# Optimization experiments

Hardware: AMD Instinct MI355X
Metric: run time of the kernel (lower is better)

## Reference

```python
import jax, jax.numpy as jnp
import numpy as np
from jax import lax

STRIDE = 1
PAD = 1  # module pads 1 on each side whenever padding != 0


def setup_inputs() -> dict:
    key = jax.random.key(0)
    kx, kw, kb = jax.random.split(key, 3)
    x = jax.random.normal(kx, (4096, 4096), dtype=jnp.float32)
    weight = jax.random.normal(kw, (15, 15), dtype=jnp.float32)
    bias = jax.random.normal(kb, (1,), dtype=jnp.float32)
    return {"x": x, "weight": weight, "bias": bias}


def reference(x, weight, bias):
    # Single-channel 2D cross-correlation with constant zero padding of 1 and
    # stride STRIDE, plus a scalar bias. lax.conv_general_dilated computes
    # correlation (no kernel flip), matching the torch corr2d loop exactly.
    out = lax.conv_general_dilated(
        x[None, None, :, :],          # NCHW, N=C=1
        weight[None, None, :, :],      # OIHW, O=I=1
        window_strides=(STRIDE, STRIDE),
        padding=[(PAD, PAD), (PAD, PAD)],
        dimension_numbers=("NCHW", "OIHW", "NCHW"),
    )[0, 0]
    return out + bias[0]
```

## Files before the change

### kernel.cpp

```cpp
#include <hip/hip_runtime.h>

#define IN_N   4096
#define OW     4084
#define KS     15
#define TILE   64
#define XROWS  78
#define XS     88
#define TILES  4
#define NBX    64
#define NBY    16
#define NRT    64

typedef __attribute__((ext_vector_type(8))) short     v8s;
typedef __attribute__((ext_vector_type(8))) _Float16  v8h;
typedef __attribute__((ext_vector_type(4))) float     v4f;
typedef __attribute__((ext_vector_type(2))) float     v2f;
typedef __attribute__((ext_vector_type(4))) unsigned  v4u;

__global__ void build_B(const float* __restrict__ w, unsigned short* __restrict__ Bg) {
    int ky = blockIdx.x;
    int e  = threadIdx.x;
    int n = e & 15, quad = e >> 4;
    unsigned short vals[8];
    #pragma unroll
    for (int j = 0; j < 8; ++j) {
        int d = quad * 8 + j - 1 - n;
        _Float16 h = (_Float16)0.0f;
        if (d >= 0 && d < KS) h = (_Float16)w[ky * KS + d];
        union { _Float16 hh; unsigned short u; } cv; cv.hh = h;
        vals[j] = cv.u;
    }
    *(v8s*)(&Bg[(ky * 64 + e) * 8]) = *(const v8s*)vals;
}

__device__ __forceinline__ unsigned pk(float a, float b) {
    return __builtin_bit_cast(unsigned, __builtin_amdgcn_cvt_pkrtz(a, b));
}

__device__ __forceinline__ void stage_direct(
    const float* __restrict__ x, unsigned short* __restrict__ buf,
    int tid, int R0, int X0, bool fast)
{
    #pragma unroll
    for (int s = 0; s < 4; ++s) {
        int i = s * 256 + tid;
        if (i < XROWS * 10) {
            int row = i / 10, u = i - 10 * row;
            int gr  = R0 - 1 + row;
            int gc0 = X0 - 2 + 8 * u;
            v4u p;
            if (fast) {
                const float* xr = x + (size_t)gr * IN_N + gc0;
                v2f f0 = *(const v2f*)(xr + 0);
                v2f f1 = *(const v2f*)(xr + 2);
                v2f f2 = *(const v2f*)(xr + 4);
                v2f f3 = *(const v2f*)(xr + 6);
                p.x = pk(f0.x, f0.y); p.y = pk(f1.x, f1.y);
                p.z = pk(f2.x, f2.y); p.w = pk(f3.x, f3.y);
            } else {
                float f[8];
                #pragma unroll
                for (int j = 0; j < 8; ++j) f[j] = 0.0f;
                if ((unsigned)gr < (unsigned)IN_N) {
                    const float* xr = x + (size_t)gr * IN_N;
                    #pragma unroll
                    for (int j = 0; j < 8; ++j)
                        if ((unsigned)(gc0 + j) < (unsigned)IN_N) f[j] = xr[gc0 + j];
                }
                p.x = pk(f[0], f[1]); p.y = pk(f[2], f[3]);
                p.z = pk(f[4], f[5]); p.w = pk(f[6], f[7]);
            }
            *(v4u*)(&buf[row * XS + 8 * u]) = p;
        }
    }
}

__device__ __forceinline__ void issue_loads(
    const float* __restrict__ x, int tid, int R0, int X0, v2f L[4][4])
{
    #pragma unroll
    for (int s = 0; s < 4; ++s) {
        int i = s * 256 + tid;
        if (i < XROWS * 10) {
            int row = i / 10, u = i - 10 * row;
            const float* xr = x + (size_t)(R0 - 1 + row) * IN_N + (X0 - 2 + 8 * u);
            L[s][0] = *(const v2f*)(xr + 0);
            L[s][1] = *(const v2f*)(xr + 2);
            L[s][2] = *(const v2f*)(xr + 4);
            L[s][3] = *(const v2f*)(xr + 6);
        }
    }
}

__device__ __forceinline__ void write_held(
    unsigned short* __restrict__ buf, int tid, v2f L[4][4])
{
    #pragma unroll
    for (int s = 0; s < 4; ++s) {
        int i = s * 256 + tid;
        if (i < XROWS * 10) {
            int row = i / 10, u = i - 10 * row;
            v4u p;
            p.x = pk(L[s][0].x, L[s][0].y);
            p.y = pk(L[s][1].x, L[s][1].y);
            p.z = pk(L[s][2].x, L[s][2].y);
            p.w = pk(L[s][3].x, L[s][3].y);
            *(v4u*)(&buf[row * XS + 8 * u]) = p;
        }
    }
}

__global__ __launch_bounds__(256, 3) void conv2d_mfma8(
    const float* __restrict__ x, const unsigned short* __restrict__ Bg,
    const float* __restrict__ bias, float* __restrict__ out)
{
    __shared__ unsigned short xt[2][XROWS * XS] __attribute__((aligned(16)));
    __shared__ unsigned short Bl[KS * 64 * 8]  __attribute__((aligned(16)));

    const int tid = threadIdx.x;
    const int bx = blockIdx.x, by = blockIdx.y;
    const int X0  = bx * TILE;
    const int RT0 = by * TILES;
    const bool colInt = (bx >= 1) & (bx <= NBX - 2);

    {
        const v8s* Bgs = (const v8s*)Bg;
        v8s* Bls = (v8s*)Bl;
        #pragma unroll
        for (int s = 0; s < 4; ++s) {
            int i = s * 256 + tid;
            if (i < KS * 64) Bls[i] = Bgs[i];
        }
    }

    stage_direct(x, xt[0], tid, RT0 * TILE, X0,
                 colInt & (RT0 >= 1) & (RT0 <= NRT - 2));
    __syncthreads();

    const int lane = tid & 63;
    const int wv   = tid >> 6;
    const int m    = lane & 15;
    const int quad = lane >> 4;
    const float bv = bias[0];

    v2f L[4][4];

    #pragma unroll
    for (int t = 0; t < TILES; ++t) {
        const int RT = RT0 + t;
        const int R0 = RT * TILE;
        const unsigned short* cur = xt[t & 1];
        unsigned short* nxt = xt[(t + 1) & 1];
        const bool hasNext = (t < TILES - 1);
        const bool nFast = hasNext & colInt & ((RT + 1) <= NRT - 2);

        if (nFast) issue_loads(x, tid, (RT + 1) * TILE, X0, L);
        __builtin_amdgcn_sched_barrier(0);

        v4f acc[4];
        #pragma unroll
        for (int c = 0; c < 4; ++c) acc[c] = (v4f){0.f, 0.f, 0.f, 0.f};

        const unsigned short* arow = &cur[(wv * 16 + m) * XS + quad * 8];
        #pragma unroll
        for (int ky = 0; ky < KS; ++ky) {
            v8h bf = *(const v8h*)(&Bl[(ky * 64 + lane) * 8]);
            v8h a0 = *(const v8h*)(arow + 0);
            v8h a1 = *(const v8h*)(arow + 16);
            v8h a2 = *(const v8h*)(arow + 32);
            v8h a3 = *(const v8h*)(arow + 48);
            acc[0] = __builtin_amdgcn_mfma_f32_16x16x32_f16(a0, bf, acc[0], 0, 0, 0);
            acc[1] = __builtin_amdgcn_mfma_f32_16x16x32_f16(a1, bf, acc[1], 0, 0, 0);
            acc[2] = __builtin_amdgcn_mfma_f32_16x16x32_f16(a2, bf, acc[2], 0, 0, 0);
            acc[3] = __builtin_amdgcn_mfma_f32_16x16x32_f16(a3, bf, acc[3], 0, 0, 0);
            arow += XS;
        }

        const int orow0 = R0 + wv * 16 + quad * 4;
        const int ocol0 = X0 + m;
        if ((bx < NBX - 1) & (RT < NRT - 1)) {
            float* o0 = &out[(size_t)orow0 * OW + ocol0];
            #pragma unroll
            for (int c = 0; c < 4; ++c) {
                #pragma unroll
                for (int r = 0; r < 4; ++r)
                    o0[(size_t)r * OW + c * 16] = acc[c][r] + bv;
            }
        } else {
            #pragma unroll
            for (int c = 0; c < 4; ++c) {
                int oc = ocol0 + c * 16;
                if (oc < OW) {
                    #pragma unroll
                    for (int r = 0; r < 4; ++r) {
                        int orow = orow0 + r;
                        if (orow < OW)
                            out[(size_t)orow * OW + oc] = acc[c][r] + bv;
                    }
                }
            }
        }
        __builtin_amdgcn_sched_barrier(0);

        if (hasNext) {
            if (nFast) write_held(nxt, tid, L);
            else       stage_direct(x, nxt, tid, (RT + 1) * TILE, X0, false);
        }
        __syncthreads();
    }
}

extern "C" void kernel_launch(void* const* d_in, const int* in_sizes, int n_in,
                              void* d_out, int out_size, void* d_ws, size_t ws_size,
                              hipStream_t stream) {
    const float* x    = (const float*)d_in[0];
    const float* w    = (const float*)d_in[1];
    const float* bias = (const float*)d_in[2];
    float* out        = (float*)d_out;
    unsigned short* Bg = (unsigned short*)d_ws;

    build_B<<<dim3(KS), dim3(64), 0, stream>>>(w, Bg);
    dim3 grid(NBX, NBY);
    conv2d_mfma8<<<grid, dim3(256), 0, stream>>>(x, Bg, bias, out);
}
```

Before: 152.3 us.

## Stage next input tile via global_load_lds DMA into a raw fp32 LDS buffer

Replaces the register-held prefetch of the next input tile with direct global-to-LDS loads into a raw float buffer. After the MFMA loop, a wait and barrier are followed by converting that buffer to fp16 in the single tile buffer. Rows per block are doubled (8 tiles, half the grid) and the row loop is no longer unrolled, which lowers register pressure. The cost is extra LDS traffic, an extra barrier per tile, and less overlap because the conversion is serialized before the next compute. Occupancy drops to 2 blocks per CU.

```diff
diff --git a/kernel.cpp b/kernel.cpp
--- a/kernel.cpp
+++ b/kernel.cpp
@@ -6,15 +6,17 @@
 #define TILE   64
 #define XROWS  78
 #define XS     88
-#define TILES  4
+#define TILES  8
 #define NBX    64
-#define NBY    16
+#define NBY    8
 #define NRT    64
+#define RAWCH  98
 
 typedef __attribute__((ext_vector_type(8))) short     v8s;
 typedef __attribute__((ext_vector_type(8))) _Float16  v8h;
 typedef __attribute__((ext_vector_type(4))) float     v4f;
 typedef __attribute__((ext_vector_type(2))) float     v2f;
+typedef __attribute__((ext_vector_type(2))) unsigned  v2u;
 typedef __attribute__((ext_vector_type(4))) unsigned  v4u;
 
 __global__ void build_B(const float* __restrict__ w, unsigned short* __restrict__ Bg) {
@@ -35,6 +37,12 @@
 
 __device__ __forceinline__ unsigned pk(float a, float b) {
     return __builtin_bit_cast(unsigned, __builtin_amdgcn_cvt_pkrtz(a, b));
+}
+
+__device__ __forceinline__ void gl_lds4(const float* g, float* l) {
+    __builtin_amdgcn_global_load_lds(
+        (const __attribute__((address_space(1))) void*)g,
+        (__attribute__((address_space(3))) void*)l, 4, 0, 0);
 }
 
 __device__ __forceinline__ void stage_direct(
@@ -75,47 +83,48 @@
     }
 }
 
-__device__ __forceinline__ void issue_loads(
-    const float* __restrict__ x, int tid, int R0, int X0, v2f L[4][4])
-{
-    #pragma unroll
-    for (int s = 0; s < 4; ++s) {
-        int i = s * 256 + tid;
-        if (i < XROWS * 10) {
-            int row = i / 10, u = i - 10 * row;
-            const float* xr = x + (size_t)(R0 - 1 + row) * IN_N + (X0 - 2 + 8 * u);
-            L[s][0] = *(const v2f*)(xr + 0);
-            L[s][1] = *(const v2f*)(xr + 2);
-            L[s][2] = *(const v2f*)(xr + 4);
-            L[s][3] = *(const v2f*)(xr + 6);
-        }
-    }
-}
-
-__device__ __forceinline__ void write_held(
-    unsigned short* __restrict__ buf, int tid, v2f L[4][4])
-{
-    #pragma unroll
-    for (int s = 0; s < 4; ++s) {
-        int i = s * 256 + tid;
-        if (i < XROWS * 10) {
-            int row = i / 10, u = i - 10 * row;
-            v4u p;
-            p.x = pk(L[s][0].x, L[s][0].y);
-            p.y = pk(L[s][1].x, L[s][1].y);
-            p.z = pk(L[s][2].x, L[s][2].y);
-            p.w = pk(L[s][3].x, L[s][3].y);
-            *(v4u*)(&buf[row * XS + 8 * u]) = p;
-        }
-    }
-}
-
-__global__ __launch_bounds__(256, 3) void conv2d_mfma8(
+__device__ __forceinline__ void dma_raw(
+    const float* __restrict__ x, float* __restrict__ raw,
+    int wv, int lane, int R0n, int X0)
+{
+    const float* xb = x + (size_t)(R0n - 1) * IN_N + (X0 - 2);
+    #pragma unroll
+    for (int s = 0; s < 25; ++s) {
+        int c = s * 4 + wv;
+        if (c < RAWCH) {
+            int f = c * 64 + lane;
+            f = (f < XROWS * 80) ? f : (XROWS * 80 - 1);
+            int row = f / 80;
+            int col = f - row * 80;
+            gl_lds4(xb + (size_t)row * IN_N + col, raw + c * 64);
+        }
+    }
+}
+
+__device__ __forceinline__ void cvt_raw(
+    const float* __restrict__ raw, unsigned short* __restrict__ xt, int tid)
+{
+    #pragma unroll
+    for (int s = 0; s < 7; ++s) {
+        int e = s * 256 + tid;
+        if (e < XROWS * 20) {
+            int row = e / 20, u = e - 20 * row;
+            v4f d = *(const v4f*)(raw + e * 4);
+            v2u p;
+            p.x = pk(d.x, d.y);
+            p.y = pk(d.z, d.w);
+            *(v2u*)(&xt[row * XS + 4 * u]) = p;
+        }
+    }
+}
+
+__global__ __launch_bounds__(256, 2) void conv2d_mfma9(
     const float* __restrict__ x, const unsigned short* __restrict__ Bg,
     const float* __restrict__ bias, float* __restrict__ out)
 {
-    __shared__ unsigned short xt[2][XROWS * XS] __attribute__((aligned(16)));
-    __shared__ unsigned short Bl[KS * 64 * 8]  __attribute__((aligned(16)));
+    __shared__ float          rawf[RAWCH * 64]      __attribute__((aligned(16)));
+    __shared__ unsigned short xtile[XROWS * XS]     __attribute__((aligned(16)));
+    __shared__ unsigned short Bl[KS * 64 * 8]       __attribute__((aligned(16)));
 
     const int tid = threadIdx.x;
     const int bx = blockIdx.x, by = blockIdx.y;
@@ -133,7 +142,7 @@
         }
     }
 
-    stage_direct(x, xt[0], tid, RT0 * TILE, X0,
+    stage_direct(x, xtile, tid, RT0 * TILE, X0,
                  colInt & (RT0 >= 1) & (RT0 <= NRT - 2));
     __syncthreads();
 
@@ -143,25 +152,20 @@
     const int quad = lane >> 4;
     const float bv = bias[0];
 
-    v2f L[4][4];
-
-    #pragma unroll
+    #pragma unroll 1
     for (int t = 0; t < TILES; ++t) {
         const int RT = RT0 + t;
         const int R0 = RT * TILE;
-        const unsigned short* cur = xt[t & 1];
-        unsigned short* nxt = xt[(t + 1) & 1];
         const bool hasNext = (t < TILES - 1);
         const bool nFast = hasNext & colInt & ((RT + 1) <= NRT - 2);
 
-        if (nFast) issue_loads(x, tid, (RT + 1) * TILE, X0, L);
-        __builtin_amdgcn_sched_barrier(0);
+        if (nFast) dma_raw(x, rawf, wv, lane, (RT + 1) * TILE, X0);
 
         v4f acc[4];
         #pragma unroll
         for (int c = 0; c < 4; ++c) acc[c] = (v4f){0.f, 0.f, 0.f, 0.f};
 
-        const unsigned short* arow = &cur[(wv * 16 + m) * XS + quad * 8];
+        const unsigned short* arow = &xtile[(wv * 16 + m) * XS + quad * 8];
         #pragma unroll
         for (int ky = 0; ky < KS; ++ky) {
             v8h bf = *(const v8h*)(&Bl[(ky * 64 + lane) * 8]);
@@ -175,6 +179,9 @@
             acc[3] = __builtin_amdgcn_mfma_f32_16x16x32_f16(a3, bf, acc[3], 0, 0, 0);
             arow += XS;
         }
+
+        asm volatile("s_waitcnt vmcnt(0)" ::: "memory");
+        __syncthreads();
 
         const int orow0 = R0 + wv * 16 + quad * 4;
         const int ocol0 = X0 + m;
@@ -200,11 +207,10 @@
                 }
             }
         }
-        __builtin_amdgcn_sched_barrier(0);
 
         if (hasNext) {
-            if (nFast) write_held(nxt, tid, L);
-            else       stage_direct(x, nxt, tid, (RT + 1) * TILE, X0, false);
+            if (nFast) cvt_raw(rawf, xtile, tid);
+            else       stage_direct(x, xtile, tid, (RT + 1) * TILE, X0, false);
         }
         __syncthreads();
     }
@@ -221,5 +227,5 @@
 
     build_B<<<dim3(KS), dim3(64), 0, stream>>>(w, Bg);
     dim3 grid(NBX, NBY);
-    conv2d_mfma8<<<grid, dim3(256), 0, stream>>>(x, Bg, bias, out);
-}
+    conv2d_mfma9<<<grid, dim3(256), 0, stream>>>(x, Bg, bias, out);
+}
```

Measured after the change: 151.5 us. Within noise of the previous version (-0.5%).
